# Kernel optimization log

Hardware: AMD Instinct MI355X
Metric: run time of the kernel (lower is better)

The kernel has to match this reference:

```python
import jax, jax.numpy as jnp
import numpy as np
from itertools import permutations
from math import factorial

N_MODES = 6
BATCH = 32768

# Clements mesh mode pairs for 6 modes: alternating odd/even layers, 15 MZIs total.
def clements_mode_list(n=6):
    pairs = []
    for layer in range(n):
        start = 0 if layer % 2 == 0 else 1
        for m in range(start, n - 1, 2):
            pairs.append((m, m + 1))
    return pairs

CLEMENTS_MODES = clements_mode_list(6)            # 15 pairs
ANSATZ_MODES = [(0, 1), (2, 3), (4, 5), (1, 2), (3, 4)] * 2  # 10 pairs (0-indexed)

IN_CONFIG = [1, 1, 1, 0, 0, 0]
OUT_CONFIGS = [list(c) for c in [
    [1,1,1,0,0,0],[1,1,0,1,0,0],[1,1,0,0,1,0],[1,1,0,0,0,1],[1,0,1,1,0,0],
    [1,0,1,0,1,0],[1,0,1,0,0,1],[1,0,0,1,1,0],[1,0,0,1,0,1],[1,0,0,0,1,1],
    [0,1,1,1,0,0],[0,1,1,0,1,0],[0,1,1,0,0,1],[0,1,0,1,1,0],[0,1,0,1,0,1],
    [0,1,0,0,1,1],[0,0,1,1,1,0],[0,0,1,1,0,1],[0,0,1,0,1,1],[0,0,0,1,1,1]]]

def _expand(config):  # occupation list -> repeated mode indices
    idx = []
    for m, c in enumerate(config):
        idx += [m] * int(c)
    return idx

IN_IDX = np.array(_expand(IN_CONFIG))                       # [3]
OUT_IDX = np.array([_expand(c) for c in OUT_CONFIGS])       # [20, 3]
N_PH = IN_IDX.shape[0]                                      # 3 photons
PERMS = list(permutations(range(N_PH)))                     # 6 perms of S_3
# boson-sampling normalization: sqrt(prod(in!) * prod(out!)) per output config (all 1 here)
NORM = np.array([np.sqrt(np.prod([factorial(int(v)) for v in IN_CONFIG]) *
                         np.prod([factorial(int(v)) for v in c])) for c in OUT_CONFIGS],
                dtype=np.float32)


def calc_unitary(modes, theta, phi):
    """Chain of MZI 2x2 rotations embedded in a 6x6 identity (Clements convention)."""
    U = jnp.eye(N_MODES, dtype=jnp.complex64)
    for k, (m, n) in enumerate(modes):
        ct = jnp.cos(theta[k]).astype(jnp.complex64)
        st = jnp.sin(theta[k]).astype(jnp.complex64)
        ep = jnp.exp(1j * phi[k].astype(jnp.complex64))
        T = jnp.eye(N_MODES, dtype=jnp.complex64)
        T = T.at[m, m].set(ep * ct).at[m, n].set(-st)
        T = T.at[n, m].set(ep * st).at[n, n].set(ct)
        U = T @ U
    return U


def permanent3(M):  # M: [..., 3, 3] complex -> [...] permanent over S_3
    acc = jnp.zeros(M.shape[:-2], dtype=M.dtype)
    for p in PERMS:
        acc = acc + M[..., 0, p[0]] * M[..., 1, p[1]] * M[..., 2, p[2]]
    return acc


def setup_inputs() -> dict:
    key = jax.random.key(0)
    ks = jax.random.split(key, 7)
    return {
        "x": jax.random.normal(ks[0], (BATCH, 12), dtype=jnp.float32),
        "params": jax.random.normal(ks[1], (30,), dtype=jnp.float32),
        "output_phase": jax.random.normal(ks[2], (6,), dtype=jnp.float32),
        "param_phi": jax.random.normal(ks[3], (4,), dtype=jnp.float32),
        "param_theta": jax.random.normal(ks[4], (4,), dtype=jnp.float32),
        "input_k": jax.random.normal(ks[5], (12,), dtype=jnp.float32),
        "input_b": jax.random.normal(ks[6], (12,), dtype=jnp.float32),
    }


def reference(x, params, output_phase, param_phi, param_theta, input_k, input_b):
    B = x.shape[0]
    # Static 6x6 interferometer: phi = params[0:15], theta = params[15:30]
    start = calc_unitary(CLEMENTS_MODES, params[15:30], params[0:15])
    start = jnp.diag(jnp.exp(1j * output_phase.astype(jnp.complex64))) @ start

    # Data-reuploading ansatz angles, [B, 10] each
    xs = x * input_k + input_b
    phi = jnp.concatenate([xs[:, 0:3], jnp.broadcast_to(param_phi[0:2], (B, 2)),
                           xs[:, 6:9], jnp.broadcast_to(param_phi[2:4], (B, 2))], axis=1)
    theta = jnp.concatenate([xs[:, 3:6], jnp.broadcast_to(param_theta[0:2], (B, 2)),
                             xs[:, 9:12], jnp.broadcast_to(param_theta[2:4], (B, 2))], axis=1)

    U_ans = jax.vmap(lambda t, p: calc_unitary(ANSATZ_MODES, t, p))(theta, phi)  # [B,6,6]
    U_final = U_ans @ start                                                      # [B,6,6]

    # Boson-sampling amplitudes: permanent of [out rows, in cols] submatrix
    sub = U_final[:, OUT_IDX[:, :, None], IN_IDX[None, None, :]]  # [B, 20, 3, 3]
    amps = permanent3(sub) / jnp.asarray(NORM)                    # [B, 20] complex

    # F.normalize(p=2, dim=1, eps=1e-12) on complex vectors
    norm = jnp.sqrt(jnp.sum(jnp.abs(amps) ** 2, axis=1, keepdims=True))
    amps = amps / jnp.maximum(norm, 1e-12)
    return jnp.abs(amps)
```

## Files before the change

kernel.cpp:

```cpp
#include <hip/hip_runtime.h>
#include <math.h>


__global__ __launch_bounds__(64) void bqnn_kernel(
    const float* __restrict__ x,
    const float* __restrict__ params,
    const float* __restrict__ output_phase,
    const float* __restrict__ param_phi,
    const float* __restrict__ param_theta,
    const float* __restrict__ input_k,
    const float* __restrict__ input_b,
    float* __restrict__ out,
    int B)
{
    __shared__ float sSre[6][3], sSim[6][3];
    __shared__ float sC[4][4];
    __shared__ float sK[12], sB[12];

    if (threadIdx.x == 0) {
        const int CM[15][2] = {{0,1},{2,3},{4,5},{1,2},{3,4},
                               {0,1},{2,3},{4,5},{1,2},{3,4},
                               {0,1},{2,3},{4,5},{1,2},{3,4}};
        float Vre[6][3], Vim[6][3];
        #pragma unroll
        for (int r = 0; r < 6; ++r)
            #pragma unroll
            for (int c = 0; c < 3; ++c) { Vre[r][c] = (r == c) ? 1.f : 0.f; Vim[r][c] = 0.f; }
        for (int k = 0; k < 15; ++k) {
            float ct, st, epr, epi;
            __sincosf(params[15 + k], &st, &ct);
            __sincosf(params[k],      &epi, &epr);
            int m = CM[k][0], n = CM[k][1];
            #pragma unroll
            for (int c = 0; c < 3; ++c) {
                float ar = Vre[m][c], ai = Vim[m][c];
                float br = Vre[n][c], bi = Vim[n][c];
                float tr = epr * ar - epi * ai;
                float ti = epr * ai + epi * ar;
                Vre[m][c] = ct * tr - st * br;
                Vim[m][c] = ct * ti - st * bi;
                Vre[n][c] = st * tr + ct * br;
                Vim[n][c] = st * ti + ct * bi;
            }
        }
        #pragma unroll
        for (int r = 0; r < 6; ++r) {
            float pr, pi;
            __sincosf(output_phase[r], &pi, &pr);
            #pragma unroll
            for (int c = 0; c < 3; ++c) {
                sSre[r][c] = pr * Vre[r][c] - pi * Vim[r][c];
                sSim[r][c] = pr * Vim[r][c] + pi * Vre[r][c];
            }
        }
        #pragma unroll
        for (int j = 0; j < 4; ++j) {
            float ct, st, epr, epi;
            __sincosf(param_theta[j], &st, &ct);
            __sincosf(param_phi[j],   &epi, &epr);
            sC[j][0] = ct; sC[j][1] = st; sC[j][2] = epr; sC[j][3] = epi;
        }
        #pragma unroll
        for (int i = 0; i < 12; ++i) { sK[i] = input_k[i]; sB[i] = input_b[i]; }
    }
    __syncthreads();

    int b = blockIdx.x * blockDim.x + threadIdx.x;
    if (b >= B) return;

    const float4* xp = reinterpret_cast<const float4*>(x + (size_t)b * 12);
    float4 a0 = xp[0], a1 = xp[1], a2 = xp[2];
    float xs[12] = {a0.x, a0.y, a0.z, a0.w, a1.x, a1.y, a1.z, a1.w, a2.x, a2.y, a2.z, a2.w};
    #pragma unroll
    for (int i = 0; i < 12; ++i) xs[i] = xs[i] * sK[i] + sB[i];

    float ct[10], st[10], epr[10], epi[10];
    __sincosf(xs[3],  &st[0], &ct[0]);  __sincosf(xs[0], &epi[0], &epr[0]);
    __sincosf(xs[4],  &st[1], &ct[1]);  __sincosf(xs[1], &epi[1], &epr[1]);
    __sincosf(xs[5],  &st[2], &ct[2]);  __sincosf(xs[2], &epi[2], &epr[2]);
    ct[3] = sC[0][0]; st[3] = sC[0][1]; epr[3] = sC[0][2]; epi[3] = sC[0][3];
    ct[4] = sC[1][0]; st[4] = sC[1][1]; epr[4] = sC[1][2]; epi[4] = sC[1][3];
    __sincosf(xs[9],  &st[5], &ct[5]);  __sincosf(xs[6], &epi[5], &epr[5]);
    __sincosf(xs[10], &st[6], &ct[6]);  __sincosf(xs[7], &epi[6], &epr[6]);
    __sincosf(xs[11], &st[7], &ct[7]);  __sincosf(xs[8], &epi[7], &epr[7]);
    ct[8] = sC[2][0]; st[8] = sC[2][1]; epr[8] = sC[2][2]; epi[8] = sC[2][3];
    ct[9] = sC[3][0]; st[9] = sC[3][1]; epr[9] = sC[3][2]; epi[9] = sC[3][3];

    float Vre[6][3], Vim[6][3];
    #pragma unroll
    for (int r = 0; r < 6; ++r)
        #pragma unroll
        for (int c = 0; c < 3; ++c) { Vre[r][c] = sSre[r][c]; Vim[r][c] = sSim[r][c]; }

    const int AM[10][2] = {{0,1},{2,3},{4,5},{1,2},{3,4},{0,1},{2,3},{4,5},{1,2},{3,4}};
    #pragma unroll
    for (int k = 0; k < 10; ++k) {
        int m = AM[k][0], n = AM[k][1];
        #pragma unroll
        for (int c = 0; c < 3; ++c) {
            float ar = Vre[m][c], ai = Vim[m][c];
            float br = Vre[n][c], bi = Vim[n][c];
            float tr = epr[k] * ar - epi[k] * ai;
            float ti = epr[k] * ai + epi[k] * ar;
            Vre[m][c] = ct[k] * tr - st[k] * br;
            Vim[m][c] = ct[k] * ti - st[k] * bi;
            Vre[n][c] = st[k] * tr + ct[k] * br;
            Vim[n][c] = st[k] * ti + ct[k] * bi;
        }
    }

    const int PR[10][2] = {{1,2},{1,3},{1,4},{1,5},{2,3},{2,4},{2,5},{3,4},{3,5},{4,5}};
    float q01r[10], q01i[10], q02r[10], q02i[10], q12r[10], q12i[10];
    #pragma unroll
    for (int p = 0; p < 10; ++p) {
        int i = PR[p][0], j = PR[p][1];
        q01r[p] = (Vre[i][0]*Vre[j][1] - Vim[i][0]*Vim[j][1]) + (Vre[i][1]*Vre[j][0] - Vim[i][1]*Vim[j][0]);
        q01i[p] = (Vre[i][0]*Vim[j][1] + Vim[i][0]*Vre[j][1]) + (Vre[i][1]*Vim[j][0] + Vim[i][1]*Vre[j][0]);
        q02r[p] = (Vre[i][0]*Vre[j][2] - Vim[i][0]*Vim[j][2]) + (Vre[i][2]*Vre[j][0] - Vim[i][2]*Vim[j][0]);
        q02i[p] = (Vre[i][0]*Vim[j][2] + Vim[i][0]*Vre[j][2]) + (Vre[i][2]*Vim[j][0] + Vim[i][2]*Vre[j][0]);
        q12r[p] = (Vre[i][1]*Vre[j][2] - Vim[i][1]*Vim[j][2]) + (Vre[i][2]*Vre[j][1] - Vim[i][2]*Vim[j][1]);
        q12i[p] = (Vre[i][1]*Vim[j][2] + Vim[i][1]*Vre[j][2]) + (Vre[i][2]*Vim[j][1] + Vim[i][2]*Vre[j][1]);
    }

    const int TA[20] = {0,0,0,0,0,0,0,0,0,0, 1,1,1,1,1,1, 2,2,2, 3};
    const int TP[20] = {0,1,2,3,4,5,6,7,8,9, 4,5,6,7,8,9, 7,8,9, 9};
    float sq[20];
    float ssum = 0.f;
    #pragma unroll
    for (int t = 0; t < 20; ++t) {
        int a = TA[t], p = TP[t];
        float pr = (Vre[a][0]*q12r[p] - Vim[a][0]*q12i[p])
                 + (Vre[a][1]*q02r[p] - Vim[a][1]*q02i[p])
                 + (Vre[a][2]*q01r[p] - Vim[a][2]*q01i[p]);
        float pi = (Vre[a][0]*q12i[p] + Vim[a][0]*q12r[p])
                 + (Vre[a][1]*q02i[p] + Vim[a][1]*q02r[p])
                 + (Vre[a][2]*q01i[p] + Vim[a][2]*q01r[p]);
        sq[t] = pr * pr + pi * pi;
        ssum += sq[t];
    }
    float inv = 1.f / fmaxf(sqrtf(ssum), 1e-12f);
    float res[20];
    #pragma unroll
    for (int t = 0; t < 20; ++t) res[t] = sqrtf(sq[t]) * inv;

    float4* op = reinterpret_cast<float4*>(out + (size_t)b * 20);
    op[0] = make_float4(res[0],  res[1],  res[2],  res[3]);
    op[1] = make_float4(res[4],  res[5],  res[6],  res[7]);
    op[2] = make_float4(res[8],  res[9],  res[10], res[11]);
    op[3] = make_float4(res[12], res[13], res[14], res[15]);
    op[4] = make_float4(res[16], res[17], res[18], res[19]);
}

extern "C" void kernel_launch(void* const* d_in, const int* in_sizes, int n_in,
                              void* d_out, int out_size, void* d_ws, size_t ws_size,
                              hipStream_t stream) {
    const float* x            = (const float*)d_in[0];
    const float* params       = (const float*)d_in[1];
    const float* output_phase = (const float*)d_in[2];
    const float* param_phi    = (const float*)d_in[3];
    const float* param_theta  = (const float*)d_in[4];
    const float* input_k      = (const float*)d_in[5];
    const float* input_b      = (const float*)d_in[6];
    int B = in_sizes[0] / 12;

    int block = 64;
    int grid = (B + block - 1) / block;
    bqnn_kernel<<<grid, block, 0, stream>>>(x, params, output_phase, param_phi,
                                            param_theta, input_k, input_b,
                                            (float*)d_out, B);
}
```

Before: 12.62 us.

## Parallelize per-block sincos prologue across lanes and recompute start unitary per thread

Instead of thread 0 serially computing the 15-MZI start unitary and trig constants while the other lanes wait, 44 lanes each compute one sincos into shared memory. After the barrier every thread rebuilds the 6x3 start matrix redundantly from those values. The x load is issued before the barrier so its latency overlaps the prologue, and out-of-range threads clamp their index instead of returning early. The trade is extra per-thread FMA work (15 MZIs) in exchange for a much shorter serial critical path before the barrier; rsqrt replaces sqrt plus divide.

Result: faster. 11.99 us (-5.0%).

```diff
diff --git a/kernel.cpp b/kernel.cpp
--- a/kernel.cpp
+++ b/kernel.cpp
@@ -13,84 +13,79 @@
     float* __restrict__ out,
     int B)
 {
-    __shared__ float sSre[6][3], sSim[6][3];
-    __shared__ float sC[4][4];
-    __shared__ float sK[12], sB[12];
+    __shared__ float sc[88];
+    int lane = threadIdx.x;
+    int b = blockIdx.x * 64 + lane;
+    int bl = (b < B) ? b : (B - 1);
 
-    if (threadIdx.x == 0) {
-        const int CM[15][2] = {{0,1},{2,3},{4,5},{1,2},{3,4},
-                               {0,1},{2,3},{4,5},{1,2},{3,4},
-                               {0,1},{2,3},{4,5},{1,2},{3,4}};
-        float Vre[6][3], Vim[6][3];
-        #pragma unroll
-        for (int r = 0; r < 6; ++r)
-            #pragma unroll
-            for (int c = 0; c < 3; ++c) { Vre[r][c] = (r == c) ? 1.f : 0.f; Vim[r][c] = 0.f; }
-        for (int k = 0; k < 15; ++k) {
-            float ct, st, epr, epi;
-            __sincosf(params[15 + k], &st, &ct);
-            __sincosf(params[k],      &epi, &epr);
-            int m = CM[k][0], n = CM[k][1];
-            #pragma unroll
-            for (int c = 0; c < 3; ++c) {
-                float ar = Vre[m][c], ai = Vim[m][c];
-                float br = Vre[n][c], bi = Vim[n][c];
-                float tr = epr * ar - epi * ai;
-                float ti = epr * ai + epi * ar;
-                Vre[m][c] = ct * tr - st * br;
-                Vim[m][c] = ct * ti - st * bi;
-                Vre[n][c] = st * tr + ct * br;
-                Vim[n][c] = st * ti + ct * bi;
-            }
-        }
-        #pragma unroll
-        for (int r = 0; r < 6; ++r) {
-            float pr, pi;
-            __sincosf(output_phase[r], &pi, &pr);
-            #pragma unroll
-            for (int c = 0; c < 3; ++c) {
-                sSre[r][c] = pr * Vre[r][c] - pi * Vim[r][c];
-                sSim[r][c] = pr * Vim[r][c] + pi * Vre[r][c];
-            }
-        }
-        #pragma unroll
-        for (int j = 0; j < 4; ++j) {
-            float ct, st, epr, epi;
-            __sincosf(param_theta[j], &st, &ct);
-            __sincosf(param_phi[j],   &epi, &epr);
-            sC[j][0] = ct; sC[j][1] = st; sC[j][2] = epr; sC[j][3] = epi;
-        }
-        #pragma unroll
-        for (int i = 0; i < 12; ++i) { sK[i] = input_k[i]; sB[i] = input_b[i]; }
+    const float4* xp = reinterpret_cast<const float4*>(x + (size_t)bl * 12);
+    float4 a0 = xp[0], a1 = xp[1], a2 = xp[2];
+
+    if (lane < 44) {
+        float arg;
+        if      (lane < 15) arg = params[15 + lane];
+        else if (lane < 30) arg = params[lane - 15];
+        else if (lane < 36) arg = output_phase[lane - 30];
+        else if (lane < 40) arg = param_theta[lane - 36];
+        else                arg = param_phi[lane - 40];
+        float s, c;
+        __sincosf(arg, &s, &c);
+        sc[2 * lane]     = s;
+        sc[2 * lane + 1] = c;
     }
     __syncthreads();
 
-    int b = blockIdx.x * blockDim.x + threadIdx.x;
-    if (b >= B) return;
+    const int CM[15][2] = {{0,1},{2,3},{4,5},{1,2},{3,4},
+                           {0,1},{2,3},{4,5},{1,2},{3,4},
+                           {0,1},{2,3},{4,5},{1,2},{3,4}};
+    float Vre[6][3], Vim[6][3];
+    #pragma unroll
+    for (int r = 0; r < 6; ++r)
+        #pragma unroll
+        for (int c = 0; c < 3; ++c) { Vre[r][c] = (r == c) ? 1.f : 0.f; Vim[r][c] = 0.f; }
+    #pragma unroll
+    for (int k = 0; k < 15; ++k) {
+        float pst = sc[2 * k],        pct = sc[2 * k + 1];
+        float pei = sc[2 * (15 + k)], per = sc[2 * (15 + k) + 1];
+        int m = CM[k][0], n = CM[k][1];
+        #pragma unroll
+        for (int c = 0; c < 3; ++c) {
+            float ar = Vre[m][c], ai = Vim[m][c];
+            float br = Vre[n][c], bi = Vim[n][c];
+            float tr = per * ar - pei * ai;
+            float ti = per * ai + pei * ar;
+            Vre[m][c] = pct * tr - pst * br;
+            Vim[m][c] = pct * ti - pst * bi;
+            Vre[n][c] = pst * tr + pct * br;
+            Vim[n][c] = pst * ti + pct * bi;
+        }
+    }
+    #pragma unroll
+    for (int r = 0; r < 6; ++r) {
+        float pi = sc[2 * (30 + r)], pr = sc[2 * (30 + r) + 1];
+        #pragma unroll
+        for (int c = 0; c < 3; ++c) {
+            float vr = Vre[r][c], vi = Vim[r][c];
+            Vre[r][c] = pr * vr - pi * vi;
+            Vim[r][c] = pr * vi + pi * vr;
+        }
+    }
 
-    const float4* xp = reinterpret_cast<const float4*>(x + (size_t)b * 12);
-    float4 a0 = xp[0], a1 = xp[1], a2 = xp[2];
     float xs[12] = {a0.x, a0.y, a0.z, a0.w, a1.x, a1.y, a1.z, a1.w, a2.x, a2.y, a2.z, a2.w};
     #pragma unroll
-    for (int i = 0; i < 12; ++i) xs[i] = xs[i] * sK[i] + sB[i];
+    for (int i = 0; i < 12; ++i) xs[i] = xs[i] * input_k[i] + input_b[i];
 
     float ct[10], st[10], epr[10], epi[10];
     __sincosf(xs[3],  &st[0], &ct[0]);  __sincosf(xs[0], &epi[0], &epr[0]);
     __sincosf(xs[4],  &st[1], &ct[1]);  __sincosf(xs[1], &epi[1], &epr[1]);
     __sincosf(xs[5],  &st[2], &ct[2]);  __sincosf(xs[2], &epi[2], &epr[2]);
-    ct[3] = sC[0][0]; st[3] = sC[0][1]; epr[3] = sC[0][2]; epi[3] = sC[0][3];
-    ct[4] = sC[1][0]; st[4] = sC[1][1]; epr[4] = sC[1][2]; epi[4] = sC[1][3];
+    st[3] = sc[2*36]; ct[3] = sc[2*36+1];  epi[3] = sc[2*40]; epr[3] = sc[2*40+1];
+    st[4] = sc[2*37]; ct[4] = sc[2*37+1];  epi[4] = sc[2*41]; epr[4] = sc[2*41+1];
     __sincosf(xs[9],  &st[5], &ct[5]);  __sincosf(xs[6], &epi[5], &epr[5]);
     __sincosf(xs[10], &st[6], &ct[6]);  __sincosf(xs[7], &epi[6], &epr[6]);
     __sincosf(xs[11], &st[7], &ct[7]);  __sincosf(xs[8], &epi[7], &epr[7]);
-    ct[8] = sC[2][0]; st[8] = sC[2][1]; epr[8] = sC[2][2]; epi[8] = sC[2][3];
-    ct[9] = sC[3][0]; st[9] = sC[3][1]; epr[9] = sC[3][2]; epi[9] = sC[3][3];
-
-    float Vre[6][3], Vim[6][3];
-    #pragma unroll
-    for (int r = 0; r < 6; ++r)
-        #pragma unroll
-        for (int c = 0; c < 3; ++c) { Vre[r][c] = sSre[r][c]; Vim[r][c] = sSim[r][c]; }
+    st[8] = sc[2*38]; ct[8] = sc[2*38+1];  epi[8] = sc[2*42]; epr[8] = sc[2*42+1];
+    st[9] = sc[2*39]; ct[9] = sc[2*39+1];  epi[9] = sc[2*43]; epr[9] = sc[2*43+1];
 
     const int AM[10][2] = {{0,1},{2,3},{4,5},{1,2},{3,4},{0,1},{2,3},{4,5},{1,2},{3,4}};
     #pragma unroll
@@ -138,17 +133,19 @@
         sq[t] = pr * pr + pi * pi;
         ssum += sq[t];
     }
-    float inv = 1.f / fmaxf(sqrtf(ssum), 1e-12f);
-    float res[20];
-    #pragma unroll
-    for (int t = 0; t < 20; ++t) res[t] = sqrtf(sq[t]) * inv;
+    float inv = rsqrtf(fmaxf(ssum, 1e-24f));
 
-    float4* op = reinterpret_cast<float4*>(out + (size_t)b * 20);
-    op[0] = make_float4(res[0],  res[1],  res[2],  res[3]);
-    op[1] = make_float4(res[4],  res[5],  res[6],  res[7]);
-    op[2] = make_float4(res[8],  res[9],  res[10], res[11]);
-    op[3] = make_float4(res[12], res[13], res[14], res[15]);
-    op[4] = make_float4(res[16], res[17], res[18], res[19]);
+    if (b < B) {
+        float res[20];
+        #pragma unroll
+        for (int t = 0; t < 20; ++t) res[t] = sqrtf(sq[t]) * inv;
+        float4* op = reinterpret_cast<float4*>(out + (size_t)b * 20);
+        op[0] = make_float4(res[0],  res[1],  res[2],  res[3]);
+        op[1] = make_float4(res[4],  res[5],  res[6],  res[7]);
+        op[2] = make_float4(res[8],  res[9],  res[10], res[11]);
+        op[3] = make_float4(res[12], res[13], res[14], res[15]);
+        op[4] = make_float4(res[16], res[17], res[18], res[19]);
+    }
 }
 
 extern "C" void kernel_launch(void* const* d_in, const int* in_sizes, int n_in,
```
